# Optimization experiments

Measured on AMD Instinct MI355X. Metric: run time of the kernel, lower is better.

Reference implementation:

```python
import jax, jax.numpy as jnp
import numpy as np

NUM_HEADS = 16

def setup_inputs() -> dict:
    key = jax.random.key(0)
    k1, k2, k3, k4 = jax.random.split(key, 4)
    B, S, D = 4, 4096, 2048
    scale = 1.0 / np.sqrt(D)
    return {
        "x": jax.random.normal(k1, (B, S, D), dtype=jnp.float32),
        "W_q": jax.random.normal(k2, (D, D), dtype=jnp.float32) * scale,
        "W_kv": jax.random.normal(k3, (D, D), dtype=jnp.float32) * scale,
        "W_o": jax.random.normal(k4, (D, D), dtype=jnp.float32) * scale,
    }

def _l2_normalize_complex(z):
    # torch.norm(z, dim=-1, keepdim=True) for complex: sqrt(sum |z|^2)
    n = jnp.sqrt(jnp.sum(jnp.abs(z) ** 2, axis=-1, keepdims=True))
    return z / n

def reference(x, W_q, W_kv, W_o):
    B, S, D = x.shape
    H = NUM_HEADS
    hd = D // H
    # Linear (no bias), torch convention: x @ W.T
    q = (x @ W_q.T).reshape(B, S, H, hd)
    kv = (x @ W_kv.T).reshape(B, S, H, hd)
    # HRR binding: FFT along head dim
    qf = jnp.fft.fft(q, axis=-1)
    kvf = jnp.fft.fft(kv, axis=-1)
    qf = _l2_normalize_complex(qf)
    kvf = _l2_normalize_complex(kvf)
    # causal=True: cumulative sum of bound key-values over sequence
    kvf = jnp.cumsum(kvf, axis=1)
    qv = qf * kvf
    values_hat = jnp.fft.ifft(qv, axis=-1).real.astype(x.dtype)
    values_hat = values_hat.reshape(B, S, D)
    return values_hat @ W_o.T
```

## Files before the change

kernel.cpp:

```cpp
#include <hip/hip_runtime.h>
#include <hip/hip_bf16.h>


typedef unsigned short u16;
typedef unsigned int u32;
typedef __attribute__((ext_vector_type(8))) short short8;
typedef __attribute__((ext_vector_type(4))) float f32x4;

__device__ __forceinline__ float bf2f(u16 u) {
  u32 x = ((u32)u) << 16;
  float f; __builtin_memcpy(&f, &x, 4); return f;
}
__device__ __forceinline__ u16 f2bf(float f) {
  __hip_bfloat16 h = __float2bfloat16(f);
  u16 u; __builtin_memcpy(&u, &h, 2); return u;
}
__device__ __forceinline__ u32 pack2(float a, float b) {
  return (u32)f2bf(a) | ((u32)f2bf(b) << 16);
}

#define GLD16(gp, lp)                                                        \
  __builtin_amdgcn_global_load_lds(                                          \
      (const __attribute__((address_space(1))) void*)(gp),                   \
      (__attribute__((address_space(3))) void*)(lp), 16, 0, 0)

__device__ __forceinline__ unsigned ldsoff(const void* p) {
  return (unsigned)(size_t)(const __attribute__((address_space(3))) char*)p;
}

#define DSR(dst, ad, im)                                                     \
  asm volatile("ds_read_b128 %0, %1 offset:%c2"                              \
               : "=v"(dst) : "v"(ad), "i"(im))

#define MFMA_PRE()                                                           \
  __builtin_amdgcn_s_barrier();                                              \
  asm volatile("s_waitcnt lgkmcnt(0)");                                      \
  __builtin_amdgcn_sched_barrier(0);                                         \
  __builtin_amdgcn_s_setprio(1)

#define MFMA_POST()                                                          \
  __builtin_amdgcn_sched_barrier(0);                                         \
  __builtin_amdgcn_s_setprio(0);                                             \
  __builtin_amdgcn_s_barrier()

template <int EPI>
__global__ __launch_bounds__(512, 2) void gemm256(
    const u16* __restrict__ A, const u16* __restrict__ B, void* __restrict__ C,
    int N, int K) {
  __shared__ alignas(1024) char smem[131072];
  const int NT = K >> 6;
  const int ntn = N >> 8;
  const int nwg = gridDim.x;
  int wg = blockIdx.x;
  wg = (wg & 7) * (nwg >> 3) + (wg >> 3);
  const int bm = wg / ntn, bn = wg % ntn;
  const long rowBase = (long)bm << 8, colBase = (long)bn << 8;

  const int tid = threadIdx.x;
  const int w = tid >> 6, lane = tid & 63;
  const int quad = lane >> 4, l16 = lane & 15;
  const int wm = w >> 2, wn = w & 3;

  const int grow = w * 8 + (lane >> 3);
  const int gcol = ((lane & 7) * 8) ^ ((lane >> 4) << 4);
  const u16* pa[2][2];
  const u16* pb[2][2];
#pragma unroll
  for (int h = 0; h < 2; h++)
#pragma unroll
    for (int r = 0; r < 2; r++) {
      pa[h][r] = A + (rowBase + h * 128 + r * 64 + grow) * (long)K + gcol;
      pb[h][r] = B + (colBase + h * 128 + r * 64 + grow) * (long)K + gcol;
    }
  char* ldsA = smem;
  char* ldsB = smem + 65536;

#define STG_A(v, h)                                                          \
  do {                                                                       \
    char* d_ = ldsA + (((v)&1) << 15) + ((h) << 14) + (w << 10);             \
    GLD16(pa[h][0] + (long)(v) * 64, d_);                                    \
    GLD16(pa[h][1] + (long)(v) * 64, d_ + 8192);                             \
  } while (0)
#define STG_B(v, h)                                                          \
  do {                                                                       \
    char* d_ = ldsB + (((v)&1) << 15) + ((h) << 14) + (w << 10);             \
    GLD16(pb[h][0] + (long)(v) * 64, d_);                                    \
    GLD16(pb[h][1] + (long)(v) * 64, d_ + 8192);                             \
  } while (0)

  const int cb0 = (quad << 4) ^ (((l16 >> 1) & 3) << 5);
  const int cb1 = cb0 ^ 64;
  const unsigned bA0 = ldsoff(ldsA + (wm * 128 + l16) * 128) + cb0;
  const unsigned bA1 = bA0 ^ 64;
  const unsigned bB0 = ldsoff(ldsB + (wn * 64 + l16) * 128) + cb0;
  const unsigned bB1 = bB0 ^ 64;
  (void)cb1;

  short8 a_[8], bl[4], bh[4];
  f32x4 acc[8][4] = {};

  STG_A(0, 0); STG_A(0, 1); STG_B(0, 0); STG_B(0, 1);
  STG_B(1, 0); STG_B(1, 1);
  asm volatile("s_waitcnt vmcnt(4)");
  __builtin_amdgcn_s_barrier();

#define RUN_TILE(uu, SA_, SB_, WAITSTMT)                                     \
  do {                                                                       \
    const unsigned bsel = ((uu) & 1) << 15;                                  \
    const unsigned aA0 = bA0 ^ bsel, aA1 = bA1 ^ bsel;                       \
    const unsigned aB0 = bB0 ^ bsel, aB1 = bB1 ^ bsel;                       \
     \
    _Pragma("unroll") for (int i = 0; i < 4; i++) {                          \
      DSR(a_[2*i],   aA0, i * 2048);                                         \
      DSR(a_[2*i+1], aA1, i * 2048);                                         \
    }                                                                        \
    _Pragma("unroll") for (int j = 0; j < 2; j++) {                          \
      DSR(bl[2*j],   aB0, j * 2048);                                         \
      DSR(bl[2*j+1], aB1, j * 2048);                                         \
    }                                                                        \
    if (SA_) STG_A((uu) + 1, 0);                                             \
    MFMA_PRE();                                                              \
    _Pragma("unroll") for (int i = 0; i < 4; i++)                            \
      _Pragma("unroll") for (int j = 0; j < 2; j++) {                        \
        acc[i][j] = __builtin_amdgcn_mfma_f32_16x16x32_bf16(a_[2*i],   bl[2*j],   acc[i][j], 0, 0, 0); \
        acc[i][j] = __builtin_amdgcn_mfma_f32_16x16x32_bf16(a_[2*i+1], bl[2*j+1], acc[i][j], 0, 0, 0); \
      }                                                                      \
    MFMA_POST();                                                             \
            \
    _Pragma("unroll") for (int j = 0; j < 2; j++) {                          \
      DSR(bh[2*j],   aB0, (j + 2) * 2048);                                   \
      DSR(bh[2*j+1], aB1, (j + 2) * 2048);                                   \
    }                                                                        \
    if (SA_) STG_A((uu) + 1, 1);                                             \
    MFMA_PRE();                                                              \
    _Pragma("unroll") for (int i = 0; i < 4; i++)                            \
      _Pragma("unroll") for (int j = 0; j < 2; j++) {                        \
        acc[i][j+2] = __builtin_amdgcn_mfma_f32_16x16x32_bf16(a_[2*i],   bh[2*j],   acc[i][j+2], 0, 0, 0); \
        acc[i][j+2] = __builtin_amdgcn_mfma_f32_16x16x32_bf16(a_[2*i+1], bh[2*j+1], acc[i][j+2], 0, 0, 0); \
      }                                                                      \
    MFMA_POST();                                                             \
            \
    _Pragma("unroll") for (int i = 0; i < 4; i++) {                          \
      DSR(a_[2*i],   aA0, (i + 4) * 2048);                                   \
      DSR(a_[2*i+1], aA1, (i + 4) * 2048);                                   \
    }                                                                        \
    if (SB_) STG_B((uu) + 2, 0);                                             \
    MFMA_PRE();                                                              \
    _Pragma("unroll") for (int i = 0; i < 4; i++)                            \
      _Pragma("unroll") for (int j = 0; j < 2; j++) {                        \
        acc[i+4][j] = __builtin_amdgcn_mfma_f32_16x16x32_bf16(a_[2*i],   bl[2*j],   acc[i+4][j], 0, 0, 0); \
        acc[i+4][j] = __builtin_amdgcn_mfma_f32_16x16x32_bf16(a_[2*i+1], bl[2*j+1], acc[i+4][j], 0, 0, 0); \
      }                                                                      \
    MFMA_POST();                                                             \
         \
    if (SB_) STG_B((uu) + 2, 1);                                             \
    MFMA_PRE();                                                              \
    _Pragma("unroll") for (int i = 0; i < 4; i++)                            \
      _Pragma("unroll") for (int j = 0; j < 2; j++) {                        \
        acc[i+4][j+2] = __builtin_amdgcn_mfma_f32_16x16x32_bf16(a_[2*i],   bh[2*j],   acc[i+4][j+2], 0, 0, 0); \
        acc[i+4][j+2] = __builtin_amdgcn_mfma_f32_16x16x32_bf16(a_[2*i+1], bh[2*j+1], acc[i+4][j+2], 0, 0, 0); \
      }                                                                      \
    __builtin_amdgcn_sched_barrier(0);                                       \
    __builtin_amdgcn_s_setprio(0);                                           \
    WAITSTMT;                                                                \
    __builtin_amdgcn_s_barrier();                                            \
  } while (0)

  for (int u = 0; u < NT - 2; ++u) {
    RUN_TILE(u, true, true, asm volatile("s_waitcnt vmcnt(4)"));
  }
  RUN_TILE(NT - 2, true, false, asm volatile("s_waitcnt vmcnt(0)"));
  RUN_TILE(NT - 1, false, false, (void)0);
#undef RUN_TILE
#undef STG_A
#undef STG_B

  asm volatile("" ::: "memory");

  float scl[8][4];
#pragma unroll
  for (int i = 0; i < 8; i++)
#pragma unroll
    for (int r = 0; r < 4; r++) scl[i][r] = 1.0f;

  if (EPI == 2) {
    float* ssb = (float*)smem;
    __syncthreads();
#pragma unroll
    for (int i = 0; i < 8; i++)
#pragma unroll
      for (int r = 0; r < 4; r++) {
        float s = 0.f;
#pragma unroll
        for (int j = 0; j < 4; j++) { float v = acc[i][j][r]; s += v * v; }
        s += __shfl_xor(s, 1); s += __shfl_xor(s, 2);
        s += __shfl_xor(s, 4); s += __shfl_xor(s, 8);
        if (l16 == 0) ssb[((wm * 128 + i * 16 + quad * 4 + r) << 2) + wn] = s;
      }
    __syncthreads();
#pragma unroll
    for (int i = 0; i < 8; i++)
#pragma unroll
      for (int r = 0; r < 4; r++) {
        int row = wm * 128 + i * 16 + quad * 4 + r;
        float s = ssb[(row << 2) + (wn & 2)] + ssb[(row << 2) + (wn & 2) + 1];
        scl[i][r] = rsqrtf(128.0f * s);
      }
  }

#pragma unroll
  for (int i = 0; i < 8; i++) {
#pragma unroll
    for (int j = 0; j < 4; j++) {
      long row0 = rowBase + wm * 128 + i * 16 + quad * 4;
      long col = colBase + wn * 64 + j * 16 + l16;
#pragma unroll
      for (int r = 0; r < 4; r++) {
        float v = acc[i][j][r] * scl[i][r];
        long off = (row0 + r) * (long)N + col;
        if (EPI == 0) ((float*)C)[off] = v;
        else          ((u16*)C)[off] = f2bf(v);
      }
    }
  }
}

template <int EPI, bool FOLD>
__global__ __launch_bounds__(256, 2) void gemm_bt(
    const u16* __restrict__ A, const u16* __restrict__ B, void* __restrict__ C,
    int M, int N, int K, int lda) {
  const int ntiles = N >> 7;
  const int bid = blockIdx.x;
  const int bm = bid / ntiles, bn = bid % ntiles;
  const long rowBase = (long)bm * 128, colBase = (long)bn * 128;
  const long aOff = FOLD ? colBase : 0;
  const long bRowBase = FOLD ? 0 : colBase;

  __shared__ u16 As[128 * 32];
  __shared__ u16 Bs[128 * 32];
  __shared__ float ssbuf[128][2];

  const int tid = threadIdx.x;
  const int wave = tid >> 6, lane = tid & 63;
  const int quad = lane >> 4, l16 = lane & 15;
  const int waveRow = (wave >> 1) * 64, waveCol = (wave & 1) * 64;

  const int srow = lane >> 2, scol = (lane & 3) * 8;
  const u16* pa = A + (rowBase + wave * 32 + srow) * (long)lda + aOff + scol;
  const u16* pb = B + (bRowBase + wave * 32 + srow) * (long)K + scol;
  u16* lA0 = &As[(wave * 32) * 32];
  u16* lA1 = &As[(wave * 32 + 16) * 32];
  u16* lB0 = &Bs[(wave * 32) * 32];
  u16* lB1 = &Bs[(wave * 32 + 16) * 32];

  f32x4 acc[4][4] = {};

  for (int kt = 0; kt < K; kt += 32) {
    GLD16(pa + kt, lA0);
    GLD16(pa + kt + 16 * (long)lda, lA1);
    GLD16(pb + kt, lB0);
    GLD16(pb + kt + 16 * (long)K, lB1);
    __syncthreads();

    short8 af[4], bfr[4];
#pragma unroll
    for (int i = 0; i < 4; i++)
      af[i] = *(const short8*)&As[(waveRow + i * 16 + l16) * 32 + quad * 8];
#pragma unroll
    for (int j = 0; j < 4; j++)
      bfr[j] = *(const short8*)&Bs[(waveCol + j * 16 + l16) * 32 + quad * 8];
#pragma unroll
    for (int i = 0; i < 4; i++)
#pragma unroll
      for (int j = 0; j < 4; j++)
        acc[i][j] = __builtin_amdgcn_mfma_f32_16x16x32_bf16(af[i], bfr[j], acc[i][j], 0, 0, 0);
    __syncthreads();
  }

  float scl[4][4];
#pragma unroll
  for (int i = 0; i < 4; i++)
#pragma unroll
    for (int r = 0; r < 4; r++) scl[i][r] = 1.0f;

  if (EPI == 2) {
#pragma unroll
    for (int i = 0; i < 4; i++) {
#pragma unroll
      for (int r = 0; r < 4; r++) {
        float s = 0.f;
#pragma unroll
        for (int j = 0; j < 4; j++) { float v = acc[i][j][r]; s += v * v; }
#pragma unroll
        for (int m = 1; m < 16; m <<= 1) s += __shfl_xor(s, m);
        if (l16 == 0) ssbuf[waveRow + i * 16 + quad * 4 + r][wave & 1] = s;
      }
    }
    __syncthreads();
#pragma unroll
    for (int i = 0; i < 4; i++)
#pragma unroll
      for (int r = 0; r < 4; r++) {
        int row = waveRow + i * 16 + quad * 4 + r;
        scl[i][r] = rsqrtf(128.0f * (ssbuf[row][0] + ssbuf[row][1]));
      }
  }

#pragma unroll
  for (int i = 0; i < 4; i++) {
#pragma unroll
    for (int j = 0; j < 4; j++) {
      long row0 = rowBase + waveRow + i * 16 + quad * 4;
      long col = colBase + waveCol + j * 16 + l16;
#pragma unroll
      for (int r = 0; r < 4; r++) {
        float v = acc[i][j][r] * scl[i][r];
        long off = (row0 + r) * (long)N + col;
        if (EPI == 0) ((float*)C)[off] = v;
        else          ((u16*)C)[off] = f2bf(v);
      }
    }
  }
}

__global__ __launch_bounds__(256) void cast_f2b(const float* __restrict__ in,
                                                u16* __restrict__ out, int n4) {
  int i = blockIdx.x * 256 + threadIdx.x;
  if (i >= n4) return;
  float4 v = ((const float4*)in)[i];
  ushort4 u;
  u.x = f2bf(v.x); u.y = f2bf(v.y); u.z = f2bf(v.z); u.w = f2bf(v.w);
  ((ushort4*)out)[i] = u;
}

__global__ __launch_bounds__(256) void init_mats(u16* __restrict__ CSp,
                                                 u16* __restrict__ W2pT) {
  int idx = blockIdx.x * 256 + threadIdx.x;
  const float PI64 = 3.14159265358979323846f / 64.0f;
  if (idx < 16384) {
    int p = idx >> 7, n = idx & 127;
    int k = p >> 1;
    float v;
    if (p == 1) v = (n & 1) ? -1.f : 1.f;
    else {
      int t = (k * n) & 127;
      float ang = (float)t * PI64;
      v = (p & 1) ? -sinf(ang) : cosf(ang);
    }
    CSp[p * 128 + n] = f2bf(v);
  } else {
    int r = idx - 16384;
    int p = r >> 7, d = r & 127;
    int k = p >> 1;
    float v;
    if (p == 0) v = 1.0f / 128.0f;
    else if (p == 1) v = ((d & 1) ? -1.f : 1.f) / 128.0f;
    else {
      int t = (k * d) & 127;
      float ang = (float)t * PI64;
      v = ((p & 1) ? -2.f * sinf(ang) : 2.f * cosf(ang)) / 128.0f;
    }
    W2pT[p * 128 + d] = f2bf(v);
  }
}

__global__ __launch_bounds__(64) void scan_chunksum(const u16* __restrict__ F,
                                                    float* __restrict__ part) {
  int blk = blockIdx.x;
  int c = blk & 63, bh = blk >> 6;
  int h = bh & 15, b = bh >> 4;
  int l = threadIdx.x;
  float s0 = 0.f, s1 = 0.f;
  for (int t = c * 64; t < c * 64 + 64; ++t) {
    u32 u = ((const u32*)(F + ((long)(b * 4096 + t) * 32 + 16 + h) * 128))[l];
    s0 += bf2f((u16)(u & 0xffff));
    s1 += bf2f((u16)(u >> 16));
  }
  float2 w; w.x = s0; w.y = s1;
  ((float2*)part)[(long)blk * 64 + l] = w;
}

__global__ __launch_bounds__(128) void scan_exclusive(float* __restrict__ part) {
  int bh = blockIdx.x;
  int j = threadIdx.x;
  float run = 0.f;
  for (int c = 0; c < 64; ++c) {
    long idx = ((long)(bh * 64 + c)) * 128 + j;
    float v = part[idx];
    part[idx] = run;
    run += v;
  }
}

__global__ __launch_bounds__(64) void scan_main(const u16* __restrict__ F,
                                                u16* __restrict__ QV,
                                                const float* __restrict__ part) {
  int blk = blockIdx.x;
  int c = blk & 63, bh = blk >> 6;
  int h = bh & 15, b = bh >> 4;
  int l = threadIdx.x;
  float2 cc = ((const float2*)part)[(long)blk * 64 + l];
  float cr = cc.x, ci = cc.y;
  for (int t = c * 64; t < c * 64 + 64; ++t) {
    long m = (long)(b * 4096 + t);
    u32 ku = ((const u32*)(F + (m * 32 + 16 + h) * 128))[l];
    u32 qu = ((const u32*)(F + (m * 32 + h) * 128))[l];
    float kr = bf2f((u16)(ku & 0xffff)), ki = bf2f((u16)(ku >> 16));
    float qr = bf2f((u16)(qu & 0xffff)), qi = bf2f((u16)(qu >> 16));
    cr += kr; ci += ki;
    float vr, vi;
    if (l == 0) { vr = qr * cr; vi = qi * ci; }
    else { vr = qr * cr - qi * ci; vi = qr * ci + qi * cr; }
    ((u32*)(QV + (m * 16 + h) * 128))[l] = pack2(vr, vi);
  }
}

extern "C" void kernel_launch(void* const* d_in, const int* in_sizes, int n_in,
                              void* d_out, int out_size, void* d_ws, size_t ws_size,
                              hipStream_t stream) {
  const float* x   = (const float*)d_in[0];
  const float* Wq  = (const float*)d_in[1];
  const float* Wkv = (const float*)d_in[2];
  const float* Wo  = (const float*)d_in[3];
  float* out = (float*)d_out;

  const long M1 = 16384;
  const long D = 2048;
  const long R = M1 * 16;
  const long XE = M1 * D;
  const long WE = D * D;

  char* ws = (char*)d_ws;
  u16* qkh  = (u16*)(ws);
  u16* F    = (u16*)(ws + 134217728);
  u16* xb   = (u16*)(ws + 268435456);
  u16* wqkb = (u16*)(ws + 335544320);
  u16* wob  = (u16*)(ws + 352321536);
  u16* wo2  = (u16*)(ws + 360710144);
  u16* CSp  = (u16*)(ws + 369098752);
  u16* W2pT = (u16*)(ws + 369131520);
  float* part = (float*)(ws + 369164288);
  u16* QV = qkh;

  cast_f2b<<<(int)(XE / 4 / 256), 256, 0, stream>>>(x, xb, (int)(XE / 4));
  cast_f2b<<<(int)(WE / 4 / 256), 256, 0, stream>>>(Wq, wqkb, (int)(WE / 4));
  cast_f2b<<<(int)(WE / 4 / 256), 256, 0, stream>>>(Wkv, wqkb + WE, (int)(WE / 4));
  cast_f2b<<<(int)(WE / 4 / 256), 256, 0, stream>>>(Wo, wob, (int)(WE / 4));
  init_mats<<<128, 256, 0, stream>>>(CSp, W2pT);

  gemm_bt<1, true><<<16 * 16, 256, 0, stream>>>(wob, W2pT, wo2, 2048, 2048, 128, 2048);

  gemm256<2><<<(int)((M1 / 256) * (4096 / 256)), 512, 0, stream>>>(
      xb, wqkb, qkh, 4096, (int)D);

  gemm_bt<1, false><<<(int)(2 * R / 128), 256, 0, stream>>>(
      qkh, CSp, F, (int)(2 * R), 128, 128, 128);

  scan_chunksum<<<64 * 64, 64, 0, stream>>>(F, part);
  scan_exclusive<<<64, 128, 0, stream>>>(part);
  scan_main<<<64 * 64, 64, 0, stream>>>(F, QV, part);

  gemm256<0><<<(int)((M1 / 256) * (D / 256)), 512, 0, stream>>>(
      QV, wo2, out, (int)D, (int)D);
}
```

Baseline: 734.4 us.

## Software-pipeline GEMM MFMA quadrants with split A registers and partial LDS waits

Splits the A fragment registers into low and high halves so the last MFMA quadrant of a tile can be deferred and run during the next tile's LDS reads. It also replaces full lgkmcnt(0) waits with partial counts so MFMAs start before all fragment reads finish. Global-load addressing is recomputed from base pointers instead of precomputed pointer arrays, which frees registers. The cost is more VGPRs for the extra A buffer, which risks spills at the 512-thread, 2-block launch bound, plus more delicate wait-count correctness.

```diff
diff --git a/kernel.cpp b/kernel.cpp
--- a/kernel.cpp
+++ b/kernel.cpp
@@ -32,16 +32,9 @@
   asm volatile("ds_read_b128 %0, %1 offset:%c2"                              \
                : "=v"(dst) : "v"(ad), "i"(im))
 
-#define MFMA_PRE()                                                           \
-  __builtin_amdgcn_s_barrier();                                              \
-  asm volatile("s_waitcnt lgkmcnt(0)");                                      \
-  __builtin_amdgcn_sched_barrier(0);                                         \
-  __builtin_amdgcn_s_setprio(1)
-
-#define MFMA_POST()                                                          \
-  __builtin_amdgcn_sched_barrier(0);                                         \
-  __builtin_amdgcn_s_setprio(0);                                             \
-  __builtin_amdgcn_s_barrier()
+#define MM2(ACCE, X0, X1, Y0, Y1)                                            \
+  ACCE = __builtin_amdgcn_mfma_f32_16x16x32_bf16(X0, Y0, ACCE, 0, 0, 0);     \
+  ACCE = __builtin_amdgcn_mfma_f32_16x16x32_bf16(X1, Y1, ACCE, 0, 0, 0)
 
 template <int EPI>
 __global__ __launch_bounds__(512, 2) void gemm256(
@@ -63,40 +56,32 @@
 
   const int grow = w * 8 + (lane >> 3);
   const int gcol = ((lane & 7) * 8) ^ ((lane >> 4) << 4);
-  const u16* pa[2][2];
-  const u16* pb[2][2];
-#pragma unroll
-  for (int h = 0; h < 2; h++)
-#pragma unroll
-    for (int r = 0; r < 2; r++) {
-      pa[h][r] = A + (rowBase + h * 128 + r * 64 + grow) * (long)K + gcol;
-      pb[h][r] = B + (colBase + h * 128 + r * 64 + grow) * (long)K + gcol;
-    }
+  const long voff = (long)grow * K + gcol;
+  const u16* Abase = A + rowBase * (long)K;
+  const u16* Bbase = B + colBase * (long)K;
   char* ldsA = smem;
   char* ldsB = smem + 65536;
 
 #define STG_A(v, h)                                                          \
   do {                                                                       \
     char* d_ = ldsA + (((v)&1) << 15) + ((h) << 14) + (w << 10);             \
-    GLD16(pa[h][0] + (long)(v) * 64, d_);                                    \
-    GLD16(pa[h][1] + (long)(v) * 64, d_ + 8192);                             \
+    GLD16(Abase + ((h) * 128L) * K + (long)(v) * 64 + voff, d_);             \
+    GLD16(Abase + ((h) * 128L + 64) * K + (long)(v) * 64 + voff, d_ + 8192); \
   } while (0)
 #define STG_B(v, h)                                                          \
   do {                                                                       \
     char* d_ = ldsB + (((v)&1) << 15) + ((h) << 14) + (w << 10);             \
-    GLD16(pb[h][0] + (long)(v) * 64, d_);                                    \
-    GLD16(pb[h][1] + (long)(v) * 64, d_ + 8192);                             \
+    GLD16(Bbase + ((h) * 128L) * K + (long)(v) * 64 + voff, d_);             \
+    GLD16(Bbase + ((h) * 128L + 64) * K + (long)(v) * 64 + voff, d_ + 8192); \
   } while (0)
 
   const int cb0 = (quad << 4) ^ (((l16 >> 1) & 3) << 5);
-  const int cb1 = cb0 ^ 64;
   const unsigned bA0 = ldsoff(ldsA + (wm * 128 + l16) * 128) + cb0;
   const unsigned bA1 = bA0 ^ 64;
   const unsigned bB0 = ldsoff(ldsB + (wn * 64 + l16) * 128) + cb0;
   const unsigned bB1 = bB0 ^ 64;
-  (void)cb1;
-
-  short8 a_[8], bl[4], bh[4];
+
+  short8 aL[8], aH[8], bl[4], bh[4];
   f32x4 acc[8][4] = {};
 
   STG_A(0, 0); STG_A(0, 1); STG_B(0, 0); STG_B(0, 1);
@@ -104,74 +89,94 @@
   asm volatile("s_waitcnt vmcnt(4)");
   __builtin_amdgcn_s_barrier();
 
-#define RUN_TILE(uu, SA_, SB_, WAITSTMT)                                     \
+#define CLUSTER(BODY)                                                        \
+  __builtin_amdgcn_sched_barrier(0);                                         \
+  __builtin_amdgcn_s_setprio(1);                                             \
+  BODY                                                                       \
+  __builtin_amdgcn_s_setprio(0);                                             \
+  __builtin_amdgcn_sched_barrier(0)
+
+#define Q3P_BODY                                                             \
+  _Pragma("unroll") for (int i = 0; i < 4; i++)                              \
+    _Pragma("unroll") for (int j = 0; j < 2; j++) {                          \
+      MM2(acc[i+4][j+2], aH[2*i], aH[2*i+1], bh[2*j], bh[2*j+1]);            \
+    }
+#define Q0_BODY                                                              \
+  _Pragma("unroll") for (int i = 0; i < 4; i++)                              \
+    _Pragma("unroll") for (int j = 0; j < 2; j++) {                          \
+      MM2(acc[i][j], aL[2*i], aL[2*i+1], bl[2*j], bl[2*j+1]);                \
+    }
+#define Q1_BODY                                                              \
+  _Pragma("unroll") for (int i = 0; i < 4; i++)                              \
+    _Pragma("unroll") for (int j = 0; j < 2; j++) {                          \
+      MM2(acc[i][j+2], aL[2*i], aL[2*i+1], bh[2*j], bh[2*j+1]);              \
+    }
+#define Q2_BODY                                                              \
+  _Pragma("unroll") for (int i = 0; i < 4; i++)                              \
+    _Pragma("unroll") for (int j = 0; j < 2; j++) {                          \
+      MM2(acc[i+4][j], aH[2*i], aH[2*i+1], bl[2*j], bl[2*j+1]);              \
+    }
+
+#define RUN_TILE(uu, Q3P, SA_, SB_, WAITSTMT)                                \
   do {                                                                       \
     const unsigned bsel = ((uu) & 1) << 15;                                  \
     const unsigned aA0 = bA0 ^ bsel, aA1 = bA1 ^ bsel;                       \
     const unsigned aB0 = bB0 ^ bsel, aB1 = bB1 ^ bsel;                       \
-     \
+                        \
     _Pragma("unroll") for (int i = 0; i < 4; i++) {                          \
-      DSR(a_[2*i],   aA0, i * 2048);                                         \
-      DSR(a_[2*i+1], aA1, i * 2048);                                         \
+      DSR(aL[2*i],   aA0, i * 2048);                                         \
+      DSR(aL[2*i+1], aA1, i * 2048);                                         \
     }                                                                        \
     _Pragma("unroll") for (int j = 0; j < 2; j++) {                          \
       DSR(bl[2*j],   aB0, j * 2048);                                         \
       DSR(bl[2*j+1], aB1, j * 2048);                                         \
     }                                                                        \
     if (SA_) STG_A((uu) + 1, 0);                                             \
-    MFMA_PRE();                                                              \
-    _Pragma("unroll") for (int i = 0; i < 4; i++)                            \
-      _Pragma("unroll") for (int j = 0; j < 2; j++) {                        \
-        acc[i][j] = __builtin_amdgcn_mfma_f32_16x16x32_bf16(a_[2*i],   bl[2*j],   acc[i][j], 0, 0, 0); \
-        acc[i][j] = __builtin_amdgcn_mfma_f32_16x16x32_bf16(a_[2*i+1], bl[2*j+1], acc[i][j], 0, 0, 0); \
-      }                                                                      \
-    MFMA_POST();                                                             \
-            \
+    __builtin_amdgcn_s_barrier();                                            \
+    if (Q3P) { CLUSTER(Q3P_BODY); }                                          \
+    __builtin_amdgcn_s_barrier();                                            \
+      \
     _Pragma("unroll") for (int j = 0; j < 2; j++) {                          \
       DSR(bh[2*j],   aB0, (j + 2) * 2048);                                   \
       DSR(bh[2*j+1], aB1, (j + 2) * 2048);                                   \
     }                                                                        \
     if (SA_) STG_A((uu) + 1, 1);                                             \
-    MFMA_PRE();                                                              \
-    _Pragma("unroll") for (int i = 0; i < 4; i++)                            \
-      _Pragma("unroll") for (int j = 0; j < 2; j++) {                        \
-        acc[i][j+2] = __builtin_amdgcn_mfma_f32_16x16x32_bf16(a_[2*i],   bh[2*j],   acc[i][j+2], 0, 0, 0); \
-        acc[i][j+2] = __builtin_amdgcn_mfma_f32_16x16x32_bf16(a_[2*i+1], bh[2*j+1], acc[i][j+2], 0, 0, 0); \
-      }                                                                      \
-    MFMA_POST();                                                             \
-            \
+    __builtin_amdgcn_s_barrier();                                            \
+    asm volatile("s_waitcnt lgkmcnt(4)");                                    \
+    CLUSTER(Q0_BODY);                                                        \
+    __builtin_amdgcn_s_barrier();                                            \
+         \
     _Pragma("unroll") for (int i = 0; i < 4; i++) {                          \
-      DSR(a_[2*i],   aA0, (i + 4) * 2048);                                   \
-      DSR(a_[2*i+1], aA1, (i + 4) * 2048);                                   \
+      DSR(aH[2*i],   aA0, (i + 4) * 2048);                                   \
+      DSR(aH[2*i+1], aA1, (i + 4) * 2048);                                   \
     }                                                                        \
     if (SB_) STG_B((uu) + 2, 0);                                             \
-    MFMA_PRE();                                                              \
-    _Pragma("unroll") for (int i = 0; i < 4; i++)                            \
-      _Pragma("unroll") for (int j = 0; j < 2; j++) {                        \
-        acc[i+4][j] = __builtin_amdgcn_mfma_f32_16x16x32_bf16(a_[2*i],   bl[2*j],   acc[i+4][j], 0, 0, 0); \
-        acc[i+4][j] = __builtin_amdgcn_mfma_f32_16x16x32_bf16(a_[2*i+1], bl[2*j+1], acc[i+4][j], 0, 0, 0); \
-      }                                                                      \
-    MFMA_POST();                                                             \
-         \
+    __builtin_amdgcn_s_barrier();                                            \
+    asm volatile("s_waitcnt lgkmcnt(8)");                                    \
+    CLUSTER(Q1_BODY);                                                        \
+    __builtin_amdgcn_s_barrier();                                            \
+        \
     if (SB_) STG_B((uu) + 2, 1);                                             \
-    MFMA_PRE();                                                              \
-    _Pragma("unroll") for (int i = 0; i < 4; i++)                            \
-      _Pragma("unroll") for (int j = 0; j < 2; j++) {                        \
-        acc[i+4][j+2] = __builtin_amdgcn_mfma_f32_16x16x32_bf16(a_[2*i],   bh[2*j],   acc[i+4][j+2], 0, 0, 0); \
-        acc[i+4][j+2] = __builtin_amdgcn_mfma_f32_16x16x32_bf16(a_[2*i+1], bh[2*j+1], acc[i+4][j+2], 0, 0, 0); \
-      }                                                                      \
-    __builtin_amdgcn_sched_barrier(0);                                       \
-    __builtin_amdgcn_s_setprio(0);                                           \
+    __builtin_amdgcn_s_barrier();                                            \
+    asm volatile("s_waitcnt lgkmcnt(0)");                                    \
+    CLUSTER(Q2_BODY);                                                        \
     WAITSTMT;                                                                \
     __builtin_amdgcn_s_barrier();                                            \
   } while (0)
 
-  for (int u = 0; u < NT - 2; ++u) {
-    RUN_TILE(u, true, true, asm volatile("s_waitcnt vmcnt(4)"));
-  }
-  RUN_TILE(NT - 2, true, false, asm volatile("s_waitcnt vmcnt(0)"));
-  RUN_TILE(NT - 1, false, false, (void)0);
+  RUN_TILE(0, false, true, true, asm volatile("s_waitcnt vmcnt(4)"));
+  for (int u = 1; u < NT - 2; ++u) {
+    RUN_TILE(u, true, true, true, asm volatile("s_waitcnt vmcnt(4)"));
+  }
+  RUN_TILE(NT - 2, true, true, false, asm volatile("s_waitcnt vmcnt(0)"));
+  RUN_TILE(NT - 1, true, false, false, (void)0);
+  { Q3P_BODY }
 #undef RUN_TILE
+#undef Q3P_BODY
+#undef Q0_BODY
+#undef Q1_BODY
+#undef Q2_BODY
+#undef CLUSTER
 #undef STG_A
 #undef STG_B
 
```

Result: no change. 739.6 us (+0.7%).
